# Kernel tuning notes

Measured on AMD Instinct MI355X. Metric: run time of the kernel, lower is better.

The kernel has to match this reference:

```python
import jax, jax.numpy as jnp
import numpy as np
from jax import lax

VOCAB = 12000
EMB = 512
RNN = 512
FEATS = 4096
SEQ_LEN = 15


def setup_inputs() -> dict:
    key = jax.random.key(0)
    ks = jax.random.split(key, 10)
    B = 1024
    s = 0.05
    return {
        "img_features": jax.random.normal(ks[0], (B, FEATS), jnp.float32),
        "W_feats": jax.random.normal(ks[1], (EMB, FEATS), jnp.float32) * s,
        "b_feats": jax.random.normal(ks[2], (EMB,), jnp.float32) * s,
        "W_ih": jax.random.normal(ks[3], (4 * RNN, EMB), jnp.float32) * s,
        "W_hh": jax.random.normal(ks[4], (4 * RNN, RNN), jnp.float32) * s,
        "b_ih": jax.random.normal(ks[5], (4 * RNN,), jnp.float32) * s,
        "b_hh": jax.random.normal(ks[6], (4 * RNN,), jnp.float32) * s,
        "emb": jax.random.normal(ks[7], (VOCAB, EMB), jnp.float32) * s,
        "W_out": jax.random.normal(ks[8], (VOCAB - 2, RNN), jnp.float32) * s,
        "b_out": jax.random.normal(ks[9], (VOCAB - 2,), jnp.float32) * s,
    }


def reference(img_features, W_feats, b_feats, W_ih, W_hh, b_ih, b_hh, emb, W_out, b_out):
    B = img_features.shape[0]

    def lstm_cell(x, h, c):
        # torch.nn.LSTMCell: gates ordered i, f, g, o
        gates = x @ W_ih.T + b_ih + h @ W_hh.T + b_hh
        i, f, g, o = jnp.split(gates, 4, axis=1)
        c_new = jax.nn.sigmoid(f) * c + jax.nn.sigmoid(i) * jnp.tanh(g)
        h_new = jax.nn.sigmoid(o) * jnp.tanh(c_new)
        return h_new, c_new

    # image feature embedding + ReLU, then prime the LSTM with it
    img_vec = jax.nn.relu(img_features @ W_feats.T + b_feats)  # [B, 512]
    h = jnp.zeros((B, RNN), img_features.dtype)
    c = jnp.zeros((B, RNN), img_features.dtype)
    h, c = lstm_cell(img_vec, h, c)

    def step(carry, _):
        h, c, words = carry
        x = emb[words]                     # [B, 512] embedding lookup
        h, c = lstm_cell(x, h, c)
        logits = h @ W_out.T + b_out       # [B, VOCAB-2]
        idx = jnp.argmax(logits, axis=1).astype(jnp.int32)
        return (h, c, idx + 2), idx

    words0 = jnp.ones((B,), jnp.int32)  # START token = 1
    _, seq = lax.scan(step, (h, c, words0), None, length=SEQ_LEN)
    return seq.T  # [B, SEQ_LEN] greedy-decoded token ids
```

## Files before the change

kernel.cpp:

```cpp
#include <hip/hip_runtime.h>
#include <stdint.h>

#define BATCH  1024
#define SEQLEN 15
#define NGATE  2048
#define NVOCAB 11998
#define FEATS  4096

typedef __attribute__((ext_vector_type(8)))  short  s8v;
typedef __attribute__((ext_vector_type(16))) float  f32x16;
typedef __attribute__((ext_vector_type(8)))  unsigned short us8;

__device__ __forceinline__ unsigned short f2bf(float f) {
    unsigned u = __float_as_uint(f);
    u += 0x7FFFu + ((u >> 16) & 1u);
    return (unsigned short)(u >> 16);
}
__device__ __forceinline__ float bf2f(unsigned short h) {
    return __uint_as_float(((unsigned)h) << 16);
}
struct bfpair { unsigned short hi, lo; };
__device__ __forceinline__ bfpair split2v(float v) {
    bfpair r;
    r.hi = f2bf(v);
    r.lo = f2bf(v - bf2f(r.hi));
    return r;
}
__device__ __forceinline__ void split8(const float* __restrict__ s, us8& vh, us8& vl) {
    #pragma unroll
    for (int e = 0; e < 8; ++e) {
        bfpair q = split2v(s[e]);
        vh[e] = q.hi; vl[e] = q.lo;
    }
}

__device__ __forceinline__ void async_cp16(const void* g, void* l) {
    __builtin_amdgcn_global_load_lds(
        (const __attribute__((address_space(1))) unsigned int*)g,
        (__attribute__((address_space(3))) unsigned int*)l, 16, 0, 0);
}

__global__ void prep_wcat_blk(const float* __restrict__ W_ih, const float* __restrict__ W_hh,
                              const float* __restrict__ b_ih, const float* __restrict__ b_hh,
                              unsigned short* __restrict__ hi, unsigned short* __restrict__ lo,
                              float* __restrict__ bsum) {
    int idx = blockIdx.x * 256 + threadIdx.x;
    int kc = idx >> 11, row = idx & 2047;
    int k = kc << 3;
    const float* src = (k < 512) ? (W_ih + (size_t)row * 512 + k)
                                 : (W_hh + (size_t)row * 512 + (k - 512));
    us8 vh, vl; split8(src, vh, vl);
    *(us8*)(hi + (size_t)idx * 8) = vh;
    *(us8*)(lo + (size_t)idx * 8) = vl;
    if (idx < NGATE) bsum[idx] = b_ih[idx] + b_hh[idx];
}

__global__ void prep_blk(const float* __restrict__ src,
                         unsigned short* __restrict__ hi, unsigned short* __restrict__ lo,
                         int R, int K) {
    int row = blockIdx.x * 256 + threadIdx.x;
    if (row >= R) return;
    int kc = blockIdx.y;
    us8 vh, vl; split8(src + (size_t)row * K + (kc << 3), vh, vl);
    size_t o = ((size_t)kc * R + row) * 8;
    *(us8*)(hi + o) = vh;
    *(us8*)(lo + o) = vl;
}

template<int MODE>
__device__ __forceinline__ void mfma_blk_body(
    const unsigned short* __restrict__ Ahi, const unsigned short* __restrict__ Alo, int aRows,
    const unsigned short* __restrict__ Bhi, const unsigned short* __restrict__ Blo, int bRows,
    float* __restrict__ C, int ldc,
    int K, size_t akstride, size_t bkstride, size_t czstride,
    int bm, int bn, int kz,
    const float* __restrict__ bias, unsigned long long* __restrict__ packed)
{
    __shared__ short smem[4 * 4 * 128 * 8];
    short* sAhi = smem;
    short* sAlo = smem + 4 * 128 * 8;
    short* sBhi = smem + 2 * 4 * 128 * 8;
    short* sBlo = smem + 3 * 4 * 128 * 8;

    Ahi += (size_t)kz * akstride;  Alo += (size_t)kz * akstride;
    Bhi += (size_t)kz * bkstride;  Blo += (size_t)kz * bkstride;
    if (MODE == 0) C += (size_t)kz * czstride;

    const int tid  = threadIdx.x;
    const int lane = tid & 63, wave = tid >> 6;
    const int wr = (wave & 1) * 64, wc = (wave >> 1) * 64;
    const int col = lane & 31, kh = lane >> 5;

    f32x16 acc[2][2] = {};

    for (int k0 = 0; k0 < K; k0 += 32) {
        const int kc0 = k0 >> 3;
        __syncthreads();
        #pragma unroll
        for (int p = 0; p < 2; ++p) {
            int s    = p * 4 + wave;
            int kc_l = s >> 1, rh = s & 1;
            int rl   = rh * 64 + lane;
            int lo_  = (kc_l * 128 + rh * 64) * 8;
            size_t ga = ((size_t)(kc0 + kc_l) * aRows + (bm + rl)) * 8;
            async_cp16(Ahi + ga, sAhi + lo_);
            async_cp16(Alo + ga, sAlo + lo_);
            int brow = bn + rl; if (brow > bRows - 1) brow = bRows - 1;
            size_t gb = ((size_t)(kc0 + kc_l) * bRows + brow) * 8;
            async_cp16(Bhi + gb, sBhi + lo_);
            async_cp16(Blo + gb, sBlo + lo_);
        }
        __syncthreads();

        #pragma unroll
        for (int st = 0; st < 2; ++st) {
            int off = (2 * st + kh) * 128 * 8;
            s8v ah0 = *(const s8v*)(sAhi + off + (wr + col) * 8);
            s8v ah1 = *(const s8v*)(sAhi + off + (wr + 32 + col) * 8);
            s8v al0 = *(const s8v*)(sAlo + off + (wr + col) * 8);
            s8v al1 = *(const s8v*)(sAlo + off + (wr + 32 + col) * 8);
            s8v bh0 = *(const s8v*)(sBhi + off + (wc + col) * 8);
            s8v bh1 = *(const s8v*)(sBhi + off + (wc + 32 + col) * 8);
            s8v bl0 = *(const s8v*)(sBlo + off + (wc + col) * 8);
            s8v bl1 = *(const s8v*)(sBlo + off + (wc + 32 + col) * 8);
            acc[0][0] = __builtin_amdgcn_mfma_f32_32x32x16_bf16(ah0, bh0, acc[0][0], 0, 0, 0);
            acc[0][1] = __builtin_amdgcn_mfma_f32_32x32x16_bf16(ah0, bh1, acc[0][1], 0, 0, 0);
            acc[1][0] = __builtin_amdgcn_mfma_f32_32x32x16_bf16(ah1, bh0, acc[1][0], 0, 0, 0);
            acc[1][1] = __builtin_amdgcn_mfma_f32_32x32x16_bf16(ah1, bh1, acc[1][1], 0, 0, 0);
            acc[0][0] = __builtin_amdgcn_mfma_f32_32x32x16_bf16(ah0, bl0, acc[0][0], 0, 0, 0);
            acc[0][1] = __builtin_amdgcn_mfma_f32_32x32x16_bf16(ah0, bl1, acc[0][1], 0, 0, 0);
            acc[1][0] = __builtin_amdgcn_mfma_f32_32x32x16_bf16(ah1, bl0, acc[1][0], 0, 0, 0);
            acc[1][1] = __builtin_amdgcn_mfma_f32_32x32x16_bf16(ah1, bl1, acc[1][1], 0, 0, 0);
            acc[0][0] = __builtin_amdgcn_mfma_f32_32x32x16_bf16(al0, bh0, acc[0][0], 0, 0, 0);
            acc[0][1] = __builtin_amdgcn_mfma_f32_32x32x16_bf16(al0, bh1, acc[0][1], 0, 0, 0);
            acc[1][0] = __builtin_amdgcn_mfma_f32_32x32x16_bf16(al1, bh0, acc[1][0], 0, 0, 0);
            acc[1][1] = __builtin_amdgcn_mfma_f32_32x32x16_bf16(al1, bh1, acc[1][1], 0, 0, 0);
        }
    }

    if (MODE == 0) {
        #pragma unroll
        for (int i = 0; i < 2; ++i)
            #pragma unroll
            for (int rg = 0; rg < 4; ++rg)
                #pragma unroll
                for (int rr = 0; rr < 4; ++rr) {
                    int reg = rg * 4 + rr;
                    int m = bm + wr + i * 32 + rr + rg * 8 + kh * 4;
                    #pragma unroll
                    for (int j = 0; j < 2; ++j) {
                        int n = bn + wc + j * 32 + col;
                        if (n < bRows) C[(size_t)m * ldc + n] = acc[i][j][reg];
                    }
                }
    } else {
        #pragma unroll
        for (int i = 0; i < 2; ++i)
            #pragma unroll
            for (int rg = 0; rg < 4; ++rg)
                #pragma unroll
                for (int rr = 0; rr < 4; ++rr) {
                    int reg = rg * 4 + rr;
                    int m = bm + wr + i * 32 + rr + rg * 8 + kh * 4;
                    unsigned long long best = 0ull;
                    #pragma unroll
                    for (int j = 0; j < 2; ++j) {
                        int n = bn + wc + j * 32 + col;
                        if (n < bRows) {
                            float v = acc[i][j][reg] + bias[n];
                            unsigned int u   = __float_as_uint(v);
                            unsigned int key = (u & 0x80000000u) ? ~u : (u | 0x80000000u);
                            unsigned long long pk =
                                ((unsigned long long)key << 32) |
                                (unsigned long long)(0xFFFFFFFFu - (unsigned)n);
                            best = (pk > best) ? pk : best;
                        }
                    }
                    #pragma unroll
                    for (int sdist = 1; sdist < 32; sdist <<= 1) {
                        unsigned long long o = __shfl_xor(best, sdist, 64);
                        best = (o > best) ? o : best;
                    }
                    if (col == 0) atomicMax(&packed[m], best);
                }
    }
}

template<int PPX>
__global__ __launch_bounds__(256) void k_gemm_gates(
    const unsigned short* Ahi, const unsigned short* Alo,
    const unsigned short* Bhi, const unsigned short* Blo,
    float* C, size_t aks, size_t bks, size_t czs) {
    const int l = blockIdx.x, r = l & 7, q = l >> 3;
    const int p = r * PPX + (q >> 3);
    const int mblk = q & 7, nblk = p & 15, kz = p >> 4;
    mfma_blk_body<0>(Ahi, Alo, 1024, Bhi, Blo, NGATE, C, NGATE, 512, aks, bks, czs,
                     mblk * 128, nblk * 128, kz, nullptr, nullptr);
}
__global__ __launch_bounds__(256) void k_gemm_feats(
    const unsigned short* Ahi, const unsigned short* Alo,
    const unsigned short* Bhi, const unsigned short* Blo,
    float* C) {
    const int l = blockIdx.x, r = l & 7, q = l >> 3;
    const int p = r * 4 + (q >> 3);
    const int mblk = q & 7, nblk = p & 3, kz = p >> 2;
    mfma_blk_body<0>(Ahi, Alo, 1024, Bhi, Blo, 512, C, 512, 512,
                     (size_t)64 * 1024 * 8, (size_t)64 * 512 * 8, (size_t)1024 * 512,
                     mblk * 128, nblk * 128, kz, nullptr, nullptr);
}

__global__ __launch_bounds__(256, 3) void k_logits_argmax(
    const unsigned short* __restrict__ h_hi, const unsigned short* __restrict__ h_lo,
    const unsigned short* __restrict__ wout_hi, const unsigned short* __restrict__ wout_lo,
    const float* __restrict__ bias, unsigned long long* __restrict__ packed) {
    int mblk, nblk;
    {
        const int l = blockIdx.x, r = l & 7, q = l >> 3;
        if (q < 88) { nblk = r * 11 + (q >> 3); mblk = q & 7; }
        else        { nblk = 88 + (q - 88);     mblk = r;     }
    }
    mfma_blk_body<1>(h_hi, h_lo, 1024, wout_hi, wout_lo, NVOCAB, nullptr, 0,
                     512, 0, 0, 0, mblk * 128, nblk * 128, 0, bias, packed);
}

__global__ void feats_reduce8(const float* __restrict__ part, const float* __restrict__ bias,
                              unsigned short* __restrict__ hi, unsigned short* __restrict__ lo) {
    int idx = blockIdx.x * 256 + threadIdx.x;
    int b = idx >> 6, kc = idx & 63;
    int n = kc << 3;
    float v[8];
    #pragma unroll
    for (int e = 0; e < 8; ++e) v[e] = bias[n + e];
    #pragma unroll
    for (int z = 0; z < 8; ++z) {
        const float* s = part + (size_t)z * 1024 * 512 + (size_t)b * 512 + n;
        #pragma unroll
        for (int e = 0; e < 8; ++e) v[e] += s[e];
    }
    us8 vh, vl;
    #pragma unroll
    for (int e = 0; e < 8; ++e) {
        bfpair q = split2v(fmaxf(v[e], 0.f));
        vh[e] = q.hi; vl[e] = q.lo;
    }
    size_t o = ((size_t)kc * 1024 + b) * 8;
    *(us8*)(hi + o) = vh;
    *(us8*)(lo + o) = vl;
}

template<bool PRIME>
__global__ void lstm_pw_blk(const float* __restrict__ g0, const float* __restrict__ g1,
                            const float* __restrict__ bsum, float* __restrict__ cbuf,
                            unsigned short* __restrict__ xh_hi, unsigned short* __restrict__ xh_lo,
                            unsigned long long* __restrict__ packed,
                            int* __restrict__ out, int t) {
    int idx = blockIdx.x * 256 + threadIdx.x;
    int b = idx >> 6, j8 = idx & 63;
    int j = j8 << 3;
    const float* g = g0 + (size_t)b * NGATE;
    float v[4][8];
    #pragma unroll
    for (int gt = 0; gt < 4; ++gt) {
        const float* s = g + gt * 512 + j;
        const float* bs = bsum + gt * 512 + j;
        #pragma unroll
        for (int e = 0; e < 8; ++e) v[gt][e] = s[e] + bs[e];
    }
    if (!PRIME) {
        const float* h2 = g1 + (size_t)b * NGATE;
        #pragma unroll
        for (int gt = 0; gt < 4; ++gt) {
            const float* s = h2 + gt * 512 + j;
            #pragma unroll
            for (int e = 0; e < 8; ++e) v[gt][e] += s[e];
        }
    }
    float* cb = cbuf + (size_t)b * 512 + j;
    us8 vh, vl;
    #pragma unroll
    for (int e = 0; e < 8; ++e) {
        float si = 1.f / (1.f + expf(-v[0][e]));
        float sf = 1.f / (1.f + expf(-v[1][e]));
        float tg = tanhf(v[2][e]);
        float so = 1.f / (1.f + expf(-v[3][e]));
        float cn = PRIME ? (si * tg) : (sf * cb[e] + si * tg);
        cb[e] = cn;
        bfpair q = split2v(so * tanhf(cn));
        vh[e] = q.hi; vl[e] = q.lo;
    }
    size_t o = ((size_t)(64 + j8) * 1024 + b) * 8;
    *(us8*)(xh_hi + o) = vh;
    *(us8*)(xh_lo + o) = vl;
    if (j8 == 0) {
        if (!PRIME && t > 0) {
            unsigned long long p = packed[b];
            out[b * SEQLEN + (t - 1)] = (int)(0xFFFFFFFFu - (unsigned)(p & 0xFFFFFFFFull));
        }
        packed[b] = 0ull;
    }
}

template<int FIRST>
__global__ void gather_blk(const float* __restrict__ emb,
                           const unsigned long long* __restrict__ packed,
                           unsigned short* __restrict__ xh_hi, unsigned short* __restrict__ xh_lo) {
    int idx = blockIdx.x * 256 + threadIdx.x;
    int b = idx >> 6, kc = idx & 63;
    int word = 1;
    if (!FIRST) {
        unsigned long long p = packed[b];
        word = (int)(0xFFFFFFFFu - (unsigned)(p & 0xFFFFFFFFull)) + 2;
    }
    us8 vh, vl; split8(emb + (size_t)word * 512 + (kc << 3), vh, vl);
    size_t o = ((size_t)kc * 1024 + b) * 8;
    *(us8*)(xh_hi + o) = vh;
    *(us8*)(xh_lo + o) = vl;
}

__global__ void final_out(const unsigned long long* __restrict__ packed, int* __restrict__ out) {
    int b = blockIdx.x * 256 + threadIdx.x;
    if (b < BATCH) {
        unsigned long long p = packed[b];
        out[b * SEQLEN + (SEQLEN - 1)] = (int)(0xFFFFFFFFu - (unsigned)(p & 0xFFFFFFFFull));
    }
}

extern "C" void kernel_launch(void* const* d_in, const int* in_sizes, int n_in,
                              void* d_out, int out_size, void* d_ws, size_t ws_size,
                              hipStream_t stream) {
    const float* img     = (const float*)d_in[0];
    const float* W_feats = (const float*)d_in[1];
    const float* b_feats = (const float*)d_in[2];
    const float* W_ih    = (const float*)d_in[3];
    const float* W_hh    = (const float*)d_in[4];
    const float* b_ih    = (const float*)d_in[5];
    const float* b_hh    = (const float*)d_in[6];
    const float* emb     = (const float*)d_in[7];
    const float* W_out   = (const float*)d_in[8];
    const float* b_out   = (const float*)d_in[9];
    int* out = (int*)d_out;

    const size_t WCAT_H = (size_t)128 * 2048 * 8;
    const size_t WOUT_H = (size_t)64 * NVOCAB * 8;
    const size_t XH_H   = (size_t)128 * 1024 * 8;
    const size_t IMGV_H = (size_t)64 * 1024 * 8;

    char* p = (char*)d_ws;
    unsigned short* wcat_hi = (unsigned short*)p;  p += WCAT_H * 2;
    unsigned short* wcat_lo = (unsigned short*)p;  p += WCAT_H * 2;
    unsigned short* wout_hi = (unsigned short*)p;  p += WOUT_H * 2;
    unsigned short* wout_lo = (unsigned short*)p;  p += WOUT_H * 2;
    unsigned short* xh_hi   = (unsigned short*)p;  p += XH_H * 2;
    unsigned short* xh_lo   = (unsigned short*)p;  p += XH_H * 2;
    unsigned short* imgv_hi = (unsigned short*)p;  p += IMGV_H * 2;
    unsigned short* imgv_lo = (unsigned short*)p;  p += IMGV_H * 2;
    float* cbuf             = (float*)p;           p += (size_t)1024 * 512 * 4;
    float* bsum             = (float*)p;           p += (size_t)NGATE * 4;
    unsigned long long* packed = (unsigned long long*)p;  p += (size_t)1024 * 8;
    float* gates0           = (float*)p;           p += (size_t)1024 * NGATE * 4;
    float* gates1           = (float*)p;           p += (size_t)1024 * NGATE * 4;
    unsigned short* imgb_hi = wout_hi;
    unsigned short* imgb_lo = imgb_hi + (size_t)512 * 1024 * 8;
    unsigned short* wfb_hi  = imgb_lo + (size_t)512 * 1024 * 8;
    unsigned short* wfb_lo  = wfb_hi  + (size_t)512 * 512 * 8;
    float* partials = gates0;

    prep_wcat_blk<<<1024, 256, 0, stream>>>(W_ih, W_hh, b_ih, b_hh, wcat_hi, wcat_lo, bsum);
    prep_blk<<<dim3(4, 512), 256, 0, stream>>>(img,     imgb_hi, imgb_lo, 1024, FEATS);
    prep_blk<<<dim3(2, 512), 256, 0, stream>>>(W_feats, wfb_hi,  wfb_lo,  512,  FEATS);

    k_gemm_feats<<<256, 256, 0, stream>>>(imgb_hi, imgb_lo, wfb_hi, wfb_lo, partials);
    feats_reduce8<<<256, 256, 0, stream>>>(partials, b_feats, imgv_hi, imgv_lo);

    prep_blk<<<dim3(47, 64), 256, 0, stream>>>(W_out, wout_hi, wout_lo, NVOCAB, 512);

    k_gemm_gates<2><<<128, 256, 0, stream>>>(imgv_hi, imgv_lo, wcat_hi, wcat_lo,
                                             gates0, 0, 0, 0);
    lstm_pw_blk<true><<<256, 256, 0, stream>>>(gates0, nullptr, bsum, cbuf,
                                               xh_hi, xh_lo, packed, out, 0);

    for (int t = 0; t < SEQLEN; ++t) {
        if (t == 0) gather_blk<1><<<256, 256, 0, stream>>>(emb, packed, xh_hi, xh_lo);
        else        gather_blk<0><<<256, 256, 0, stream>>>(emb, packed, xh_hi, xh_lo);
        k_gemm_gates<4><<<256, 256, 0, stream>>>(
            xh_hi, xh_lo, wcat_hi, wcat_lo, gates0,
            (size_t)64 * 1024 * 8, (size_t)64 * 2048 * 8, (size_t)1024 * NGATE);
        lstm_pw_blk<false><<<256, 256, 0, stream>>>(gates0, gates1, bsum, cbuf,
                                                    xh_hi, xh_lo, packed, out, t);
        k_logits_argmax<<<752, 256, 0, stream>>>(
            xh_hi + (size_t)64 * 1024 * 8, xh_lo + (size_t)64 * 1024 * 8,
            wout_hi, wout_lo, b_out, packed);
    }
    final_out<<<4, 256, 0, stream>>>(packed, out);
}
```

Baseline: 1.834 ms.

## Double-buffer W_out tiles and load h directly into registers in logits kernel

The logits+argmax kernel gets its own main loop. It stages only the W_out hi/lo tiles into double-buffered shared memory using async copies, and prefetches the next k-step. The h operand fragments are read straight from global memory into registers, also one step ahead. This aims to overlap loads with MFMA work, halve shared-memory traffic for A, and drop one barrier per iteration, at the cost of more registers under the launch bound of 3 blocks per CU. The gate and feature GEMMs keep the shared body, now specialised to storing only.

Result: faster. 1.620 ms (median of 3 runs) (-11.7%).

```diff
diff --git a/kernel.cpp b/kernel.cpp
--- a/kernel.cpp
+++ b/kernel.cpp
@@ -67,14 +67,12 @@
     *(us8*)(lo + o) = vl;
 }
 
-template<int MODE>
-__device__ __forceinline__ void mfma_blk_body(
+__device__ __forceinline__ void mfma_blk_store(
     const unsigned short* __restrict__ Ahi, const unsigned short* __restrict__ Alo, int aRows,
     const unsigned short* __restrict__ Bhi, const unsigned short* __restrict__ Blo, int bRows,
     float* __restrict__ C, int ldc,
     int K, size_t akstride, size_t bkstride, size_t czstride,
-    int bm, int bn, int kz,
-    const float* __restrict__ bias, unsigned long long* __restrict__ packed)
+    int bm, int bn, int kz)
 {
     __shared__ short smem[4 * 4 * 128 * 8];
     short* sAhi = smem;
@@ -84,7 +82,7 @@
 
     Ahi += (size_t)kz * akstride;  Alo += (size_t)kz * akstride;
     Bhi += (size_t)kz * bkstride;  Blo += (size_t)kz * bkstride;
-    if (MODE == 0) C += (size_t)kz * czstride;
+    C   += (size_t)kz * czstride;
 
     const int tid  = threadIdx.x;
     const int lane = tid & 63, wave = tid >> 6;
@@ -138,52 +136,20 @@
         }
     }
 
-    if (MODE == 0) {
-        #pragma unroll
-        for (int i = 0; i < 2; ++i)
-            #pragma unroll
-            for (int rg = 0; rg < 4; ++rg)
+    #pragma unroll
+    for (int i = 0; i < 2; ++i)
+        #pragma unroll
+        for (int rg = 0; rg < 4; ++rg)
+            #pragma unroll
+            for (int rr = 0; rr < 4; ++rr) {
+                int reg = rg * 4 + rr;
+                int m = bm + wr + i * 32 + rr + rg * 8 + kh * 4;
                 #pragma unroll
-                for (int rr = 0; rr < 4; ++rr) {
-                    int reg = rg * 4 + rr;
-                    int m = bm + wr + i * 32 + rr + rg * 8 + kh * 4;
-                    #pragma unroll
-                    for (int j = 0; j < 2; ++j) {
-                        int n = bn + wc + j * 32 + col;
-                        if (n < bRows) C[(size_t)m * ldc + n] = acc[i][j][reg];
-                    }
+                for (int j = 0; j < 2; ++j) {
+                    int n = bn + wc + j * 32 + col;
+                    if (n < bRows) C[(size_t)m * ldc + n] = acc[i][j][reg];
                 }
-    } else {
-        #pragma unroll
-        for (int i = 0; i < 2; ++i)
-            #pragma unroll
-            for (int rg = 0; rg < 4; ++rg)
-                #pragma unroll
-                for (int rr = 0; rr < 4; ++rr) {
-                    int reg = rg * 4 + rr;
-                    int m = bm + wr + i * 32 + rr + rg * 8 + kh * 4;
-                    unsigned long long best = 0ull;
-                    #pragma unroll
-                    for (int j = 0; j < 2; ++j) {
-                        int n = bn + wc + j * 32 + col;
-                        if (n < bRows) {
-                            float v = acc[i][j][reg] + bias[n];
-                            unsigned int u   = __float_as_uint(v);
-                            unsigned int key = (u & 0x80000000u) ? ~u : (u | 0x80000000u);
-                            unsigned long long pk =
-                                ((unsigned long long)key << 32) |
-                                (unsigned long long)(0xFFFFFFFFu - (unsigned)n);
-                            best = (pk > best) ? pk : best;
-                        }
-                    }
-                    #pragma unroll
-                    for (int sdist = 1; sdist < 32; sdist <<= 1) {
-                        unsigned long long o = __shfl_xor(best, sdist, 64);
-                        best = (o > best) ? o : best;
-                    }
-                    if (col == 0) atomicMax(&packed[m], best);
-                }
-    }
+            }
 }
 
 template<int PPX>
@@ -194,8 +160,8 @@
     const int l = blockIdx.x, r = l & 7, q = l >> 3;
     const int p = r * PPX + (q >> 3);
     const int mblk = q & 7, nblk = p & 15, kz = p >> 4;
-    mfma_blk_body<0>(Ahi, Alo, 1024, Bhi, Blo, NGATE, C, NGATE, 512, aks, bks, czs,
-                     mblk * 128, nblk * 128, kz, nullptr, nullptr);
+    mfma_blk_store(Ahi, Alo, 1024, Bhi, Blo, NGATE, C, NGATE, 512, aks, bks, czs,
+                   mblk * 128, nblk * 128, kz);
 }
 __global__ __launch_bounds__(256) void k_gemm_feats(
     const unsigned short* Ahi, const unsigned short* Alo,
@@ -204,23 +170,126 @@
     const int l = blockIdx.x, r = l & 7, q = l >> 3;
     const int p = r * 4 + (q >> 3);
     const int mblk = q & 7, nblk = p & 3, kz = p >> 2;
-    mfma_blk_body<0>(Ahi, Alo, 1024, Bhi, Blo, 512, C, 512, 512,
-                     (size_t)64 * 1024 * 8, (size_t)64 * 512 * 8, (size_t)1024 * 512,
-                     mblk * 128, nblk * 128, kz, nullptr, nullptr);
+    mfma_blk_store(Ahi, Alo, 1024, Bhi, Blo, 512, C, 512, 512,
+                   (size_t)64 * 1024 * 8, (size_t)64 * 512 * 8, (size_t)1024 * 512,
+                   mblk * 128, nblk * 128, kz);
 }
 
 __global__ __launch_bounds__(256, 3) void k_logits_argmax(
     const unsigned short* __restrict__ h_hi, const unsigned short* __restrict__ h_lo,
     const unsigned short* __restrict__ wout_hi, const unsigned short* __restrict__ wout_lo,
-    const float* __restrict__ bias, unsigned long long* __restrict__ packed) {
+    const float* __restrict__ bias, unsigned long long* __restrict__ packed)
+{
+    __shared__ short sB[2][2][4][128][8];
+
     int mblk, nblk;
     {
         const int l = blockIdx.x, r = l & 7, q = l >> 3;
         if (q < 88) { nblk = r * 11 + (q >> 3); mblk = q & 7; }
         else        { nblk = 88 + (q - 88);     mblk = r;     }
     }
-    mfma_blk_body<1>(h_hi, h_lo, 1024, wout_hi, wout_lo, NVOCAB, nullptr, 0,
-                     512, 0, 0, 0, mblk * 128, nblk * 128, 0, bias, packed);
+
+    const int tid  = threadIdx.x;
+    const int lane = tid & 63, wave = tid >> 6;
+    const int wm = wave & 1, wn = wave >> 1;
+    const int col = lane & 31, kh = lane >> 5;
+    const int bm = mblk * 128, bn = nblk * 128;
+    const int aRows = 1024, bRows = NVOCAB;
+
+    f32x16 acc[2][2] = {};
+
+    auto stage_B = [&](int kcbase, int bufi) {
+        #pragma unroll
+        for (int p = 0; p < 4; ++p) {
+            int s = p * 4 + wave;
+            int arr = s >> 3, kc_l = (s >> 1) & 3, rh = s & 1;
+            int brow = bn + rh * 64 + lane; if (brow > bRows - 1) brow = bRows - 1;
+            size_t gb = ((size_t)(kcbase + kc_l) * bRows + brow) * 8;
+            async_cp16((arr ? wout_lo : wout_hi) + gb, &sB[bufi][arr][kc_l][rh * 64][0]);
+        }
+    };
+    auto load_A = [&](int kc0, s8v (&ah)[2][2], s8v (&al)[2][2]) {
+        #pragma unroll
+        for (int st = 0; st < 2; ++st)
+            #pragma unroll
+            for (int i = 0; i < 2; ++i) {
+                size_t ao = ((size_t)(kc0 + 2 * st + kh) * aRows
+                             + (bm + wm * 64 + i * 32 + col)) * 8;
+                ah[st][i] = *(const s8v*)(h_hi + ao);
+                al[st][i] = *(const s8v*)(h_lo + ao);
+            }
+    };
+
+    stage_B(0, 0);
+    s8v ahc[2][2], alc[2][2], ahn[2][2], aln[2][2];
+    load_A(0, ahc, alc);
+    __syncthreads();
+
+    int cur = 0;
+    for (int ks = 0; ks < 16; ++ks) {
+        if (ks + 1 < 16) {
+            stage_B((ks + 1) << 2, cur ^ 1);
+            load_A((ks + 1) << 2, ahn, aln);
+        }
+
+        #pragma unroll
+        for (int st = 0; st < 2; ++st) {
+            const int kl = 2 * st + kh;
+            #pragma unroll
+            for (int j = 0; j < 2; ++j) {
+                const s8v bh = *(const s8v*)&sB[cur][0][kl][wn * 64 + j * 32 + col][0];
+                const s8v bl = *(const s8v*)&sB[cur][1][kl][wn * 64 + j * 32 + col][0];
+                #pragma unroll
+                for (int i = 0; i < 2; ++i) {
+                    acc[i][j] = __builtin_amdgcn_mfma_f32_32x32x16_bf16(ahc[st][i], bh, acc[i][j], 0, 0, 0);
+                    acc[i][j] = __builtin_amdgcn_mfma_f32_32x32x16_bf16(ahc[st][i], bl, acc[i][j], 0, 0, 0);
+                    acc[i][j] = __builtin_amdgcn_mfma_f32_32x32x16_bf16(alc[st][i], bh, acc[i][j], 0, 0, 0);
+                }
+            }
+        }
+
+        __syncthreads();
+        cur ^= 1;
+        if (ks + 1 < 16) {
+            #pragma unroll
+            for (int st = 0; st < 2; ++st)
+                #pragma unroll
+                for (int i = 0; i < 2; ++i) {
+                    ahc[st][i] = ahn[st][i];
+                    alc[st][i] = aln[st][i];
+                }
+        }
+    }
+
+    #pragma unroll
+    for (int i = 0; i < 2; ++i)
+        #pragma unroll
+        for (int rg = 0; rg < 4; ++rg)
+            #pragma unroll
+            for (int rr = 0; rr < 4; ++rr) {
+                int reg = rg * 4 + rr;
+                int m = bm + wm * 64 + i * 32 + rr + rg * 8 + kh * 4;
+                unsigned long long best = 0ull;
+                #pragma unroll
+                for (int j = 0; j < 2; ++j) {
+                    int n = bn + wn * 64 + j * 32 + col;
+                    if (n < bRows) {
+                        float v = acc[i][j][reg] + bias[n];
+                        unsigned int u   = __float_as_uint(v);
+                        unsigned int key = (u & 0x80000000u) ? ~u : (u | 0x80000000u);
+                        unsigned long long pk =
+                            ((unsigned long long)key << 32) |
+                            (unsigned long long)(0xFFFFFFFFu - (unsigned)n);
+                        best = (pk > best) ? pk : best;
+                    }
+                }
+                #pragma unroll
+                for (int sdist = 1; sdist < 32; sdist <<= 1) {
+                    unsigned long long o = __shfl_xor(best, sdist, 64);
+                    best = (o > best) ? o : best;
+                }
+                if (col == 0) atomicMax(&packed[m], best);
+            }
 }
 
 __global__ void feats_reduce8(const float* __restrict__ part, const float* __restrict__ bias,
```

## Load logits-GEMM operands straight from global into registers, skipping LDS staging

Applied to the files above, without the earlier changes.

The logits+argmax kernel no longer goes through the shared LDS-tiled GEMM body. Each wave now loads its bf16 hi/lo fragments for h and W_out directly from global memory into registers, with the whole K=512 loop unrolled. This removes the LDS round-trip and the per-k-step __syncthreads, and lets loads be issued ahead of the MFMAs. In exchange, data is no longer reused across waves through LDS, so global/L2 traffic per block goes up, and the full unroll raises register pressure under launch_bounds(256,3).

After: 1.713 ms. 6.6% less time.

```diff
diff --git a/kernel.cpp b/kernel.cpp
--- a/kernel.cpp
+++ b/kernel.cpp
@@ -67,14 +67,12 @@
     *(us8*)(lo + o) = vl;
 }
 
-template<int MODE>
-__device__ __forceinline__ void mfma_blk_body(
+__device__ __forceinline__ void mfma_blk_store(
     const unsigned short* __restrict__ Ahi, const unsigned short* __restrict__ Alo, int aRows,
     const unsigned short* __restrict__ Bhi, const unsigned short* __restrict__ Blo, int bRows,
     float* __restrict__ C, int ldc,
     int K, size_t akstride, size_t bkstride, size_t czstride,
-    int bm, int bn, int kz,
-    const float* __restrict__ bias, unsigned long long* __restrict__ packed)
+    int bm, int bn, int kz)
 {
     __shared__ short smem[4 * 4 * 128 * 8];
     short* sAhi = smem;
@@ -84,7 +82,7 @@
 
     Ahi += (size_t)kz * akstride;  Alo += (size_t)kz * akstride;
     Bhi += (size_t)kz * bkstride;  Blo += (size_t)kz * bkstride;
-    if (MODE == 0) C += (size_t)kz * czstride;
+    C   += (size_t)kz * czstride;
 
     const int tid  = threadIdx.x;
     const int lane = tid & 63, wave = tid >> 6;
@@ -138,52 +136,20 @@
         }
     }
 
-    if (MODE == 0) {
-        #pragma unroll
-        for (int i = 0; i < 2; ++i)
+    #pragma unroll
+    for (int i = 0; i < 2; ++i)
+        #pragma unroll
+        for (int rg = 0; rg < 4; ++rg)
             #pragma unroll
-            for (int rg = 0; rg < 4; ++rg)
+            for (int rr = 0; rr < 4; ++rr) {
+                int reg = rg * 4 + rr;
+                int m = bm + wr + i * 32 + rr + rg * 8 + kh * 4;
                 #pragma unroll
-                for (int rr = 0; rr < 4; ++rr) {
-                    int reg = rg * 4 + rr;
-                    int m = bm + wr + i * 32 + rr + rg * 8 + kh * 4;
-                    #pragma unroll
-                    for (int j = 0; j < 2; ++j) {
-                        int n = bn + wc + j * 32 + col;
-                        if (n < bRows) C[(size_t)m * ldc + n] = acc[i][j][reg];
-                    }
+                for (int j = 0; j < 2; ++j) {
+                    int n = bn + wc + j * 32 + col;
+                    if (n < bRows) C[(size_t)m * ldc + n] = acc[i][j][reg];
                 }
-    } else {
-        #pragma unroll
-        for (int i = 0; i < 2; ++i)
-            #pragma unroll
-            for (int rg = 0; rg < 4; ++rg)
-                #pragma unroll
-                for (int rr = 0; rr < 4; ++rr) {
-                    int reg = rg * 4 + rr;
-                    int m = bm + wr + i * 32 + rr + rg * 8 + kh * 4;
-                    unsigned long long best = 0ull;
-                    #pragma unroll
-                    for (int j = 0; j < 2; ++j) {
-                        int n = bn + wc + j * 32 + col;
-                        if (n < bRows) {
-                            float v = acc[i][j][reg] + bias[n];
-                            unsigned int u   = __float_as_uint(v);
-                            unsigned int key = (u & 0x80000000u) ? ~u : (u | 0x80000000u);
-                            unsigned long long pk =
-                                ((unsigned long long)key << 32) |
-                                (unsigned long long)(0xFFFFFFFFu - (unsigned)n);
-                            best = (pk > best) ? pk : best;
-                        }
-                    }
-                    #pragma unroll
-                    for (int sdist = 1; sdist < 32; sdist <<= 1) {
-                        unsigned long long o = __shfl_xor(best, sdist, 64);
-                        best = (o > best) ? o : best;
-                    }
-                    if (col == 0) atomicMax(&packed[m], best);
-                }
-    }
+            }
 }
 
 template<int PPX>
@@ -194,8 +160,8 @@
     const int l = blockIdx.x, r = l & 7, q = l >> 3;
     const int p = r * PPX + (q >> 3);
     const int mblk = q & 7, nblk = p & 15, kz = p >> 4;
-    mfma_blk_body<0>(Ahi, Alo, 1024, Bhi, Blo, NGATE, C, NGATE, 512, aks, bks, czs,
-                     mblk * 128, nblk * 128, kz, nullptr, nullptr);
+    mfma_blk_store(Ahi, Alo, 1024, Bhi, Blo, NGATE, C, NGATE, 512, aks, bks, czs,
+                   mblk * 128, nblk * 128, kz);
 }
 __global__ __launch_bounds__(256) void k_gemm_feats(
     const unsigned short* Ahi, const unsigned short* Alo,
@@ -204,23 +170,94 @@
     const int l = blockIdx.x, r = l & 7, q = l >> 3;
     const int p = r * 4 + (q >> 3);
     const int mblk = q & 7, nblk = p & 3, kz = p >> 2;
-    mfma_blk_body<0>(Ahi, Alo, 1024, Bhi, Blo, 512, C, 512, 512,
-                     (size_t)64 * 1024 * 8, (size_t)64 * 512 * 8, (size_t)1024 * 512,
-                     mblk * 128, nblk * 128, kz, nullptr, nullptr);
+    mfma_blk_store(Ahi, Alo, 1024, Bhi, Blo, 512, C, 512, 512,
+                   (size_t)64 * 1024 * 8, (size_t)64 * 512 * 8, (size_t)1024 * 512,
+                   mblk * 128, nblk * 128, kz);
 }
 
 __global__ __launch_bounds__(256, 3) void k_logits_argmax(
     const unsigned short* __restrict__ h_hi, const unsigned short* __restrict__ h_lo,
     const unsigned short* __restrict__ wout_hi, const unsigned short* __restrict__ wout_lo,
-    const float* __restrict__ bias, unsigned long long* __restrict__ packed) {
+    const float* __restrict__ bias, unsigned long long* __restrict__ packed)
+{
     int mblk, nblk;
     {
         const int l = blockIdx.x, r = l & 7, q = l >> 3;
         if (q < 88) { nblk = r * 11 + (q >> 3); mblk = q & 7; }
         else        { nblk = 88 + (q - 88);     mblk = r;     }
     }
-    mfma_blk_body<1>(h_hi, h_lo, 1024, wout_hi, wout_lo, NVOCAB, nullptr, 0,
-                     512, 0, 0, 0, mblk * 128, nblk * 128, 0, bias, packed);
+
+    const int tid  = threadIdx.x;
+    const int lane = tid & 63, wave = tid >> 6;
+    const int wm = wave & 1, wn = wave >> 1;
+    const int col = lane & 31, kh = lane >> 5;
+    const int bm = mblk * 128, bn = nblk * 128;
+    const int aRows = 1024, bRows = NVOCAB;
+
+    int ar0 = bm + wm * 64 + col, ar1 = ar0 + 32;
+    int br0 = bn + wn * 64 + col;      if (br0 > bRows - 1) br0 = bRows - 1;
+    int br1 = bn + wn * 64 + 32 + col; if (br1 > bRows - 1) br1 = bRows - 1;
+
+    f32x16 acc[2][2] = {};
+
+    #pragma unroll
+    for (int ks = 0; ks < 16; ++ks) {
+        const int kc0 = ks << 2;
+        s8v ah[2][2], al[2][2], bh[2][2], bl[2][2];
+        #pragma unroll
+        for (int st = 0; st < 2; ++st) {
+            const size_t kA = (size_t)(kc0 + 2 * st + kh) * aRows;
+            const size_t kB = (size_t)(kc0 + 2 * st + kh) * bRows;
+            ah[st][0] = *(const s8v*)(h_hi + (kA + ar0) * 8);
+            ah[st][1] = *(const s8v*)(h_hi + (kA + ar1) * 8);
+            al[st][0] = *(const s8v*)(h_lo + (kA + ar0) * 8);
+            al[st][1] = *(const s8v*)(h_lo + (kA + ar1) * 8);
+            bh[st][0] = *(const s8v*)(wout_hi + (kB + br0) * 8);
+            bh[st][1] = *(const s8v*)(wout_hi + (kB + br1) * 8);
+            bl[st][0] = *(const s8v*)(wout_lo + (kB + br0) * 8);
+            bl[st][1] = *(const s8v*)(wout_lo + (kB + br1) * 8);
+        }
+        #pragma unroll
+        for (int st = 0; st < 2; ++st)
+            #pragma unroll
+            for (int j = 0; j < 2; ++j)
+                #pragma unroll
+                for (int i = 0; i < 2; ++i) {
+                    acc[i][j] = __builtin_amdgcn_mfma_f32_32x32x16_bf16(ah[st][i], bh[st][j], acc[i][j], 0, 0, 0);
+                    acc[i][j] = __builtin_amdgcn_mfma_f32_32x32x16_bf16(ah[st][i], bl[st][j], acc[i][j], 0, 0, 0);
+                    acc[i][j] = __builtin_amdgcn_mfma_f32_32x32x16_bf16(al[st][i], bh[st][j], acc[i][j], 0, 0, 0);
+                }
+    }
+
+    #pragma unroll
+    for (int i = 0; i < 2; ++i)
+        #pragma unroll
+        for (int rg = 0; rg < 4; ++rg)
+            #pragma unroll
+            for (int rr = 0; rr < 4; ++rr) {
+                int reg = rg * 4 + rr;
+                int m = bm + wm * 64 + i * 32 + rr + rg * 8 + kh * 4;
+                unsigned long long best = 0ull;
+                #pragma unroll
+                for (int j = 0; j < 2; ++j) {
+                    int n = bn + wn * 64 + j * 32 + col;
+                    if (n < bRows) {
+                        float v = acc[i][j][reg] + bias[n];
+                        unsigned int u   = __float_as_uint(v);
+                        unsigned int key = (u & 0x80000000u) ? ~u : (u | 0x80000000u);
+                        unsigned long long pk =
+                            ((unsigned long long)key << 32) |
+                            (unsigned long long)(0xFFFFFFFFu - (unsigned)n);
+                        best = (pk > best) ? pk : best;
+                    }
+                }
+                #pragma unroll
+                for (int sdist = 1; sdist < 32; sdist <<= 1) {
+                    unsigned long long o = __shfl_xor(best, sdist, 64);
+                    best = (o > best) ? o : best;
+                }
+                if (col == 0) atomicMax(&packed[m], best);
+            }
 }
 
 __global__ void feats_reduce8(const float* __restrict__ part, const float* __restrict__ bias,
```

## Add producer-consumer warp specialization with triple-buffered async loads in GEMMs

Applied to the files above, without the earlier changes.

Restructures the shared GEMM body so each block has 8 waves. Four producer waves issue async global-to-LDS copies into a 3-stage ring buffer, two stages ahead, and four consumer waves run the MFMA loop, with the two groups kept in step by barriers. This replaces the old load-then-compute loop, which had two __syncthreads per K-step and no overlap. The cost is more LDS per block (three buffers), twice the threads per block, and a K loop hard-coded to 512, which drops the K parameter.

After: 5.176 ms. 2.82x slower.

```diff
diff --git a/kernel.cpp b/kernel.cpp
--- a/kernel.cpp
+++ b/kernel.cpp
@@ -68,19 +68,15 @@
 }
 
 template<int MODE>
-__device__ __forceinline__ void mfma_blk_body(
+__device__ __forceinline__ void gemm_pc(
     const unsigned short* __restrict__ Ahi, const unsigned short* __restrict__ Alo, int aRows,
     const unsigned short* __restrict__ Bhi, const unsigned short* __restrict__ Blo, int bRows,
     float* __restrict__ C, int ldc,
-    int K, size_t akstride, size_t bkstride, size_t czstride,
+    size_t akstride, size_t bkstride, size_t czstride,
     int bm, int bn, int kz,
     const float* __restrict__ bias, unsigned long long* __restrict__ packed)
 {
-    __shared__ short smem[4 * 4 * 128 * 8];
-    short* sAhi = smem;
-    short* sAlo = smem + 4 * 128 * 8;
-    short* sBhi = smem + 2 * 4 * 128 * 8;
-    short* sBlo = smem + 3 * 4 * 128 * 8;
+    __shared__ short s3[3][4][4][128][8];
 
     Ahi += (size_t)kz * akstride;  Alo += (size_t)kz * akstride;
     Bhi += (size_t)kz * bkstride;  Blo += (size_t)kz * bkstride;
@@ -88,41 +84,66 @@
 
     const int tid  = threadIdx.x;
     const int lane = tid & 63, wave = tid >> 6;
-    const int wr = (wave & 1) * 64, wc = (wave >> 1) * 64;
+
+    if (wave >= 4) {
+        const int wp = wave - 4;
+        auto stage = [&](int t) {
+            const int kc0  = t << 2;
+            const int bufi = t % 3;
+            #pragma unroll
+            for (int p = 0; p < 8; ++p) {
+                int s = p * 4 + wp;
+                int arr = s >> 3, rem = s & 7;
+                int kc_l = rem >> 1, rh = rem & 1;
+                int row = rh * 64 + lane;
+                const unsigned short* src;
+                if (arr < 2) {
+                    size_t go = ((size_t)(kc0 + kc_l) * aRows + (bm + row)) * 8;
+                    src = (arr == 0 ? Ahi : Alo) + go;
+                } else {
+                    int brow = bn + row; if (brow > bRows - 1) brow = bRows - 1;
+                    size_t go = ((size_t)(kc0 + kc_l) * bRows + brow) * 8;
+                    src = (arr == 2 ? Bhi : Blo) + go;
+                }
+                async_cp16(src, &s3[bufi][arr][kc_l][rh * 64][0]);
+            }
+        };
+        stage(0);
+        stage(1);
+        asm volatile("s_waitcnt vmcnt(8)" ::: "memory");
+        __builtin_amdgcn_s_barrier();
+        for (int t = 0; t < 16; ++t) {
+            if (t + 2 < 16) {
+                stage(t + 2);
+                asm volatile("s_waitcnt vmcnt(8)" ::: "memory");
+            } else {
+                asm volatile("s_waitcnt vmcnt(0)" ::: "memory");
+            }
+            __builtin_amdgcn_s_barrier();
+        }
+        return;
+    }
+
+    const int wm = wave & 1, wn = wave >> 1;
     const int col = lane & 31, kh = lane >> 5;
 
     f32x16 acc[2][2] = {};
 
-    for (int k0 = 0; k0 < K; k0 += 32) {
-        const int kc0 = k0 >> 3;
-        __syncthreads();
-        #pragma unroll
-        for (int p = 0; p < 2; ++p) {
-            int s    = p * 4 + wave;
-            int kc_l = s >> 1, rh = s & 1;
-            int rl   = rh * 64 + lane;
-            int lo_  = (kc_l * 128 + rh * 64) * 8;
-            size_t ga = ((size_t)(kc0 + kc_l) * aRows + (bm + rl)) * 8;
-            async_cp16(Ahi + ga, sAhi + lo_);
-            async_cp16(Alo + ga, sAlo + lo_);
-            int brow = bn + rl; if (brow > bRows - 1) brow = bRows - 1;
-            size_t gb = ((size_t)(kc0 + kc_l) * bRows + brow) * 8;
-            async_cp16(Bhi + gb, sBhi + lo_);
-            async_cp16(Blo + gb, sBlo + lo_);
-        }
-        __syncthreads();
-
+    __syncthreads();
+
+    for (int t = 0; t < 16; ++t) {
+        const int bufi = t % 3;
         #pragma unroll
         for (int st = 0; st < 2; ++st) {
-            int off = (2 * st + kh) * 128 * 8;
-            s8v ah0 = *(const s8v*)(sAhi + off + (wr + col) * 8);
-            s8v ah1 = *(const s8v*)(sAhi + off + (wr + 32 + col) * 8);
-            s8v al0 = *(const s8v*)(sAlo + off + (wr + col) * 8);
-            s8v al1 = *(const s8v*)(sAlo + off + (wr + 32 + col) * 8);
-            s8v bh0 = *(const s8v*)(sBhi + off + (wc + col) * 8);
-            s8v bh1 = *(const s8v*)(sBhi + off + (wc + 32 + col) * 8);
-            s8v bl0 = *(const s8v*)(sBlo + off + (wc + col) * 8);
-            s8v bl1 = *(const s8v*)(sBlo + off + (wc + 32 + col) * 8);
+            const int kl = 2 * st + kh;
+            s8v ah0 = *(const s8v*)&s3[bufi][0][kl][wm * 64 +      col][0];
+            s8v ah1 = *(const s8v*)&s3[bufi][0][kl][wm * 64 + 32 + col][0];
+            s8v al0 = *(const s8v*)&s3[bufi][1][kl][wm * 64 +      col][0];
+            s8v al1 = *(const s8v*)&s3[bufi][1][kl][wm * 64 + 32 + col][0];
+            s8v bh0 = *(const s8v*)&s3[bufi][2][kl][wn * 64 +      col][0];
+            s8v bh1 = *(const s8v*)&s3[bufi][2][kl][wn * 64 + 32 + col][0];
+            s8v bl0 = *(const s8v*)&s3[bufi][3][kl][wn * 64 +      col][0];
+            s8v bl1 = *(const s8v*)&s3[bufi][3][kl][wn * 64 + 32 + col][0];
             acc[0][0] = __builtin_amdgcn_mfma_f32_32x32x16_bf16(ah0, bh0, acc[0][0], 0, 0, 0);
             acc[0][1] = __builtin_amdgcn_mfma_f32_32x32x16_bf16(ah0, bh1, acc[0][1], 0, 0, 0);
             acc[1][0] = __builtin_amdgcn_mfma_f32_32x32x16_bf16(ah1, bh0, acc[1][0], 0, 0, 0);
@@ -136,6 +157,7 @@
             acc[1][0] = __builtin_amdgcn_mfma_f32_32x32x16_bf16(al1, bh0, acc[1][0], 0, 0, 0);
             acc[1][1] = __builtin_amdgcn_mfma_f32_32x32x16_bf16(al1, bh1, acc[1][1], 0, 0, 0);
         }
+        __syncthreads();
     }
 
     if (MODE == 0) {
@@ -146,10 +168,10 @@
                 #pragma unroll
                 for (int rr = 0; rr < 4; ++rr) {
                     int reg = rg * 4 + rr;
-                    int m = bm + wr + i * 32 + rr + rg * 8 + kh * 4;
+                    int m = bm + wm * 64 + i * 32 + rr + rg * 8 + kh * 4;
                     #pragma unroll
                     for (int j = 0; j < 2; ++j) {
-                        int n = bn + wc + j * 32 + col;
+                        int n = bn + wn * 64 + j * 32 + col;
                         if (n < bRows) C[(size_t)m * ldc + n] = acc[i][j][reg];
                     }
                 }
@@ -161,11 +183,11 @@
                 #pragma unroll
                 for (int rr = 0; rr < 4; ++rr) {
                     int reg = rg * 4 + rr;
-                    int m = bm + wr + i * 32 + rr + rg * 8 + kh * 4;
+                    int m = bm + wm * 64 + i * 32 + rr + rg * 8 + kh * 4;
                     unsigned long long best = 0ull;
                     #pragma unroll
                     for (int j = 0; j < 2; ++j) {
-                        int n = bn + wc + j * 32 + col;
+                        int n = bn + wn * 64 + j * 32 + col;
                         if (n < bRows) {
                             float v = acc[i][j][reg] + bias[n];
                             unsigned int u   = __float_as_uint(v);
@@ -187,29 +209,28 @@
 }
 
 template<int PPX>
-__global__ __launch_bounds__(256) void k_gemm_gates(
+__global__ __launch_bounds__(512, 2) void k_gemm_gates(
     const unsigned short* Ahi, const unsigned short* Alo,
     const unsigned short* Bhi, const unsigned short* Blo,
     float* C, size_t aks, size_t bks, size_t czs) {
     const int l = blockIdx.x, r = l & 7, q = l >> 3;
     const int p = r * PPX + (q >> 3);
     const int mblk = q & 7, nblk = p & 15, kz = p >> 4;
-    mfma_blk_body<0>(Ahi, Alo, 1024, Bhi, Blo, NGATE, C, NGATE, 512, aks, bks, czs,
-                     mblk * 128, nblk * 128, kz, nullptr, nullptr);
-}
-__global__ __launch_bounds__(256) void k_gemm_feats(
+    gemm_pc<0>(Ahi, Alo, 1024, Bhi, Blo, NGATE, C, NGATE, aks, bks, czs,
+               mblk * 128, nblk * 128, kz, nullptr, nullptr);
+}
+__global__ __launch_bounds__(512, 2) void k_gemm_feats(
     const unsigned short* Ahi, const unsigned short* Alo,
     const unsigned short* Bhi, const unsigned short* Blo,
     float* C) {
     const int l = blockIdx.x, r = l & 7, q = l >> 3;
     const int p = r * 4 + (q >> 3);
     const int mblk = q & 7, nblk = p & 3, kz = p >> 2;
-    mfma_blk_body<0>(Ahi, Alo, 1024, Bhi, Blo, 512, C, 512, 512,
-                     (size_t)64 * 1024 * 8, (size_t)64 * 512 * 8, (size_t)1024 * 512,
-                     mblk * 128, nblk * 128, kz, nullptr, nullptr);
-}
-
-__global__ __launch_bounds__(256, 3) void k_logits_argmax(
+    gemm_pc<0>(Ahi, Alo, 1024, Bhi, Blo, 512, C, 512,
+               (size_t)64 * 1024 * 8, (size_t)64 * 512 * 8, (size_t)1024 * 512,
+               mblk * 128, nblk * 128, kz, nullptr, nullptr);
+}
+__global__ __launch_bounds__(512, 2) void k_logits_argmax(
     const unsigned short* __restrict__ h_hi, const unsigned short* __restrict__ h_lo,
     const unsigned short* __restrict__ wout_hi, const unsigned short* __restrict__ wout_lo,
     const float* __restrict__ bias, unsigned long long* __restrict__ packed) {
@@ -219,8 +240,8 @@
         if (q < 88) { nblk = r * 11 + (q >> 3); mblk = q & 7; }
         else        { nblk = 88 + (q - 88);     mblk = r;     }
     }
-    mfma_blk_body<1>(h_hi, h_lo, 1024, wout_hi, wout_lo, NVOCAB, nullptr, 0,
-                     512, 0, 0, 0, mblk * 128, nblk * 128, 0, bias, packed);
+    gemm_pc<1>(h_hi, h_lo, 1024, wout_hi, wout_lo, NVOCAB, nullptr, 0,
+               0, 0, 0, mblk * 128, nblk * 128, 0, bias, packed);
 }
 
 __global__ void feats_reduce8(const float* __restrict__ part, const float* __restrict__ bias,
@@ -369,12 +390,12 @@
     prep_blk<<<dim3(4, 512), 256, 0, stream>>>(img,     imgb_hi, imgb_lo, 1024, FEATS);
     prep_blk<<<dim3(2, 512), 256, 0, stream>>>(W_feats, wfb_hi,  wfb_lo,  512,  FEATS);
 
-    k_gemm_feats<<<256, 256, 0, stream>>>(imgb_hi, imgb_lo, wfb_hi, wfb_lo, partials);
+    k_gemm_feats<<<256, 512, 0, stream>>>(imgb_hi, imgb_lo, wfb_hi, wfb_lo, partials);
     feats_reduce8<<<256, 256, 0, stream>>>(partials, b_feats, imgv_hi, imgv_lo);
 
     prep_blk<<<dim3(47, 64), 256, 0, stream>>>(W_out, wout_hi, wout_lo, NVOCAB, 512);
 
-    k_gemm_gates<2><<<128, 256, 0, stream>>>(imgv_hi, imgv_lo, wcat_hi, wcat_lo,
+    k_gemm_gates<2><<<128, 512, 0, stream>>>(imgv_hi, imgv_lo, wcat_hi, wcat_lo,
                                              gates0, 0, 0, 0);
     lstm_pw_blk<true><<<256, 256, 0, stream>>>(gates0, nullptr, bsum, cbuf,
                                                xh_hi, xh_lo, packed, out, 0);
@@ -382,12 +403,12 @@
     for (int t = 0; t < SEQLEN; ++t) {
         if (t == 0) gather_blk<1><<<256, 256, 0, stream>>>(emb, packed, xh_hi, xh_lo);
         else        gather_blk<0><<<256, 256, 0, stream>>>(emb, packed, xh_hi, xh_lo);
-        k_gemm_gates<4><<<256, 256, 0, stream>>>(
+        k_gemm_gates<4><<<256, 512, 0, stream>>>(
             xh_hi, xh_lo, wcat_hi, wcat_lo, gates0,
             (size_t)64 * 1024 * 8, (size_t)64 * 2048 * 8, (size_t)1024 * NGATE);
         lstm_pw_blk<false><<<256, 256, 0, stream>>>(gates0, gates1, bsum, cbuf,
                                                     xh_hi, xh_lo, packed, out, t);
-        k_logits_argmax<<<752, 256, 0, stream>>>(
+        k_logits_argmax<<<752, 512, 0, stream>>>(
             xh_hi + (size_t)64 * 1024 * 8, xh_lo + (size_t)64 * 1024 * 8,
             wout_hi, wout_lo, b_out, packed);
     }
```
